# Performance work log

Measured on AMD Instinct MI355X. Metric: run time of the kernel, lower is better.

The kernel has to match this reference:

```python
import math
import jax, jax.numpy as jnp
import numpy as np

B, S, M, H = 8, 2048, 2048, 512
GH = 512  # gate_hidden
MIX_BIAS = -0.25
VARIATION_BIAS = -1.0
PRIOR_SCALE = 1.0
GATE_SCALE = 1.0
GATE_BIAS = 0.0
EPS = 1e-6


def _slerp(a, b, t, eps=EPS):
    # F.normalize semantics: x / max(||x||, eps)
    an = a / jnp.maximum(jnp.linalg.norm(a, axis=-1, keepdims=True), eps)
    bn = b / jnp.maximum(jnp.linalg.norm(b, axis=-1, keepdims=True), eps)
    dot = jnp.clip(jnp.sum(an * bn, axis=-1, keepdims=True), -1.0 + eps, 1.0 - eps)
    omega = jnp.arccos(dot)
    sin_omega = jnp.maximum(jnp.sin(omega), eps)
    t = jnp.clip(t, 0.0, 1.0)
    scale_a = jnp.sin((1.0 - t) * omega) / sin_omega
    scale_b = jnp.sin(t * omega) / sin_omega
    return scale_a * a + scale_b * b


def setup_inputs() -> dict:
    key = jax.random.key(0)
    ks = jax.random.split(key, 20)
    sc = 1.0 / math.sqrt(H)
    sc4 = 1.0 / math.sqrt(4 * H)
    scg = 1.0 / math.sqrt(GH)
    inp = {
        "query": jax.random.normal(ks[0], (B, S, H), jnp.float32),
        "global_anchor": jax.random.normal(ks[1], (B, H), jnp.float32),
        "global_memory": jax.random.normal(ks[2], (B, M, H), jnp.float32),
        "local_absolute": jax.random.normal(ks[3], (B, S, H), jnp.float32),
        "style_context": jax.random.normal(ks[4], (B, S, H), jnp.float32),
        # projection params, stored as [in, out]
        "Wq": jax.random.normal(ks[5], (H, H), jnp.float32) * sc,
        "bq": jnp.zeros((H,), jnp.float32),
        "Wk": jax.random.normal(ks[6], (H, H), jnp.float32) * sc,
        "bk": jnp.zeros((H,), jnp.float32),
        "Wv": jax.random.normal(ks[7], (H, H), jnp.float32) * sc,
        "bv": jnp.zeros((H,), jnp.float32),
        "Wo": jax.random.normal(ks[8], (H, H), jnp.float32) * sc,
        "bo": jnp.zeros((H,), jnp.float32),
        # mix gate MLP: 4H -> GH -> 1
        "Wm1": jax.random.normal(ks[9], (4 * H, GH), jnp.float32) * sc4,
        "bm1": jnp.zeros((GH,), jnp.float32),
        "Wm2": jax.random.normal(ks[10], (GH, 1), jnp.float32) * scg,
        "bm2": jnp.zeros((1,), jnp.float32),
        # variation gate MLP: 4H -> GH -> 1
        "Wg1": jax.random.normal(ks[11], (4 * H, GH), jnp.float32) * sc4,
        "bg1": jnp.zeros((GH,), jnp.float32),
        "Wg2": jax.random.normal(ks[12], (GH, 1), jnp.float32) * scg,
        "bg2": jnp.zeros((1,), jnp.float32),
    }
    return inp


def reference(query, global_anchor, global_memory, local_absolute, style_context,
              Wq, bq, Wk, bk, Wv, bv, Wo, bo,
              Wm1, bm1, Wm2, bm2, Wg1, bg1, Wg2, bg2):
    # expand anchor [B,H] -> [B,S,H]
    anchor_seq = jnp.broadcast_to(global_anchor[:, None, :], query.shape)

    q = query @ Wq + bq                      # [B,S,H]
    k = global_memory @ Wk + bk              # [B,M,H]
    v = global_memory @ Wv + bv              # [B,M,H]

    attn_logits = jnp.einsum('bsh,bmh->bsm', q, k) / math.sqrt(float(H))
    attn = jax.nn.softmax(attn_logits, axis=-1)                      # [B,S,M]
    prior_delta = (jnp.einsum('bsm,bmh->bsh', attn, v) @ Wo + bo) * PRIOR_SCALE
    prior_absolute = anchor_seq + prior_delta

    mix_in = jnp.concatenate([query, prior_absolute, local_absolute, style_context], axis=-1)
    mix_logit = jax.nn.relu(mix_in @ Wm1 + bm1) @ Wm2 + bm2          # [B,S,1]
    mix = jax.nn.sigmoid(mix_logit + MIX_BIAS)

    candidate_absolute = _slerp(prior_absolute, local_absolute, mix)

    var_in = jnp.concatenate([query, candidate_absolute, anchor_seq, style_context], axis=-1)
    variation_logit = jax.nn.relu(var_in @ Wg1 + bg1) @ Wg2 + bg2    # [B,S,1]
    variation_gate = jax.nn.sigmoid(variation_logit * GATE_SCALE + GATE_BIAS + VARIATION_BIAS)

    candidate_delta = candidate_absolute - anchor_seq
    return (attn, prior_delta, prior_absolute, mix, candidate_absolute,
            candidate_delta, variation_logit, variation_gate)
```

## Files before the change

### kernel.cpp

```cpp
#include <hip/hip_runtime.h>
#include <hip/hip_bf16.h>

typedef __hip_bfloat16 bf16;
typedef unsigned short u16;
typedef u16 u16x8 __attribute__((ext_vector_type(8)));
typedef u16 u16x4v __attribute__((ext_vector_type(4)));
typedef short bf16x8 __attribute__((ext_vector_type(8)));
typedef float f32x4 __attribute__((ext_vector_type(4)));

__device__ __forceinline__ float b2f(u16 u) {
    unsigned v = ((unsigned)u) << 16;
    float f; __builtin_memcpy(&f, &v, 4); return f;
}
__device__ __forceinline__ u16 f2u(float f) {
    bf16 h = __float2bfloat16(f);
    u16 u; __builtin_memcpy(&u, &h, 2); return u;
}
__device__ __forceinline__ float sigmoidf_(float x) { return 1.f / (1.f + expf(-x)); }
__device__ __forceinline__ void load8f(const float* __restrict__ p, float* x) {
    float4 a = *reinterpret_cast<const float4*>(p);
    float4 b = *reinterpret_cast<const float4*>(p + 4);
    x[0]=a.x; x[1]=a.y; x[2]=a.z; x[3]=a.w; x[4]=b.x; x[5]=b.y; x[6]=b.z; x[7]=b.w;
}

__device__ __forceinline__ void gld16(const void* g, void* l) {
    typedef __attribute__((address_space(1))) const unsigned int GU;
    typedef __attribute__((address_space(3))) unsigned int LU;
    __builtin_amdgcn_global_load_lds((GU*)(unsigned long long)g,
                                     (LU*)(unsigned int)(unsigned long long)l, 16, 0, 0);
}

template<int EPI, int SWZ>
__global__ __launch_bounds__(256)
void k_mfma(const bf16* __restrict__ A, long long sA, int lda,
            const bf16* __restrict__ Bt, long long sB, int ldb,
            const float* __restrict__ bias, const float* __restrict__ bias2,
            bf16* __restrict__ outb, bf16* __restrict__ outb2, long long sO,
            float* __restrict__ out1, float* __restrict__ out2,
            const float* __restrict__ anchor,
            int N, int K, float scale, int GX)
{
    __shared__ short As[4096];
    __shared__ short Bs[4096];
    const int tid = threadIdx.x;
    const int lin = blockIdx.x;
    int x, y, z;
    if constexpr (SWZ == 0) {
        z = lin & 7; const int t = lin >> 3; x = t % GX; y = t / GX;
    } else {
        const int q = (int)gridDim.x >> 3;
        const int wq = (lin & 7) * q + (lin >> 3);
        x = wq % GX; y = wq / GX; z = 0;
    }
    const int n0 = x * 128, m0 = y * 128;
    const bf16* Az = A + (long long)z * sA;
    const bf16* Bz = Bt + (long long)z * sB;
    const int lrow = tid >> 2;
    const int lcol = (tid & 3) * 8;
    const int lane = tid & 63, w = tid >> 6;
    const int wm = (w >> 1) * 64, wn = (w & 1) * 64;
    const int fr = lane & 15, fq = lane >> 4;
    char* AsW = (char*)As + w * 1024;
    char* BsW = (char*)Bs + w * 1024;

    f32x4 acc[4][4];
#pragma unroll
    for (int i = 0; i < 4; ++i)
#pragma unroll
        for (int j = 0; j < 4; ++j) acc[i][j] = f32x4{0.f, 0.f, 0.f, 0.f};

    for (int k0 = 0; k0 < K; k0 += 32) {
        const bf16* ga = Az + (long long)(m0 + lrow) * lda + (k0 + lcol);
        const bf16* gb = Bz + (long long)(n0 + lrow) * ldb + (k0 + lcol);
        gld16(ga, AsW);
        gld16(ga + 64LL * lda, AsW + 4096);
        gld16(gb, BsW);
        gld16(gb + 64LL * ldb, BsW + 4096);
        __syncthreads();

        bf16x8 af[4], bfr[4];
#pragma unroll
        for (int i = 0; i < 4; ++i)
            af[i] = *reinterpret_cast<const bf16x8*>(&As[(wm + i * 16 + fr) * 32 + fq * 8]);
#pragma unroll
        for (int j = 0; j < 4; ++j)
            bfr[j] = *reinterpret_cast<const bf16x8*>(&Bs[(wn + j * 16 + fr) * 32 + fq * 8]);
#pragma unroll
        for (int i = 0; i < 4; ++i)
#pragma unroll
            for (int j = 0; j < 4; ++j)
                acc[i][j] = __builtin_amdgcn_mfma_f32_16x16x32_bf16(af[i], bfr[j], acc[i][j], 0, 0, 0);
        __syncthreads();
    }

#pragma unroll
    for (int j = 0; j < 4; ++j) {
        const int col = n0 + wn + j * 16 + fr;
        float bv;
        if constexpr (EPI == 1) bv = (col < 512) ? bias[col] : bias2[col - 512];
        else                    bv = bias ? bias[col] : 0.f;
#pragma unroll
        for (int i = 0; i < 4; ++i) {
#pragma unroll
            for (int r = 0; r < 4; ++r) {
                const long long row = m0 + wm + i * 16 + fq * 4 + r;
                const float v = acc[i][j][r];
                if constexpr (EPI == 0) {
                    outb[(long long)z * sO + row * N + col] = __float2bfloat16(v * scale + bv);
                } else if constexpr (EPI == 1) {
                    if (col < 512) outb[row * 512 + col] = __float2bfloat16(v + bv);
                    else           outb2[row * 512 + (col - 512)] = __float2bfloat16(v + bv);
                } else {
                    const float pd = v + bv;
                    const float pa = pd + anchor[(row >> 11) * 512 + col];
                    out1[row * N + col] = pd;
                    out2[row * N + col] = pa;
                    outb[row * N + col] = __float2bfloat16(pa);
                }
            }
        }
    }
}

__global__ __launch_bounds__(256)
void k_softmax_b(bf16* __restrict__ Lb, float* __restrict__ attn)
{
    __shared__ float redm[4], reds[4];
    const long long row = blockIdx.x;
    bf16* lp = Lb + row * 2048;
    float* ap = attn + row * 2048;
    const int tid = threadIdx.x;

    u16x8 u = *reinterpret_cast<const u16x8*>(lp + tid * 8);
    float x[8];
    float mx = -1e30f;
#pragma unroll
    for (int j = 0; j < 8; ++j) { x[j] = b2f(u[j]); mx = fmaxf(mx, x[j]); }
#pragma unroll
    for (int off = 32; off; off >>= 1) mx = fmaxf(mx, __shfl_xor(mx, off));
    if ((tid & 63) == 0) redm[tid >> 6] = mx;
    __syncthreads();
    mx = fmaxf(fmaxf(redm[0], redm[1]), fmaxf(redm[2], redm[3]));

    float s = 0.f;
#pragma unroll
    for (int j = 0; j < 8; ++j) { x[j] = __expf(x[j] - mx); s += x[j]; }
#pragma unroll
    for (int off = 32; off; off >>= 1) s += __shfl_xor(s, off);
    if ((tid & 63) == 0) reds[tid >> 6] = s;
    __syncthreads();
    const float inv = 1.f / (reds[0] + reds[1] + reds[2] + reds[3]);

    u16x8 ob;
#pragma unroll
    for (int j = 0; j < 8; ++j) { x[j] *= inv; ob[j] = f2u(x[j]); }
    *reinterpret_cast<float4*>(ap + tid * 8)     = make_float4(x[0], x[1], x[2], x[3]);
    *reinterpret_cast<float4*>(ap + tid * 8 + 4) = make_float4(x[4], x[5], x[6], x[7]);
    *reinterpret_cast<u16x8*>(lp + tid * 8) = ob;
}

__global__ __launch_bounds__(256)
void k_cat(const bf16* __restrict__ s0b, const bf16* __restrict__ s1b,
           const bf16* __restrict__ s2b, const bf16* __restrict__ s3b,
           int mode2,
           const bf16* __restrict__ Bt, const float* __restrict__ bias,
           const float* __restrict__ w2, float* __restrict__ part)
{
    __shared__ short As[4096];
    __shared__ short Bs[4096];
    __shared__ float pl[128][2];
    const int tid = threadIdx.x;
    const int lin = blockIdx.x;
    const int q = (int)gridDim.x >> 3;
    const int wq = (lin & 7) * q + (lin >> 3);
    const int xt = wq & 3;
    const int n0 = xt * 128, m0 = (wq >> 2) * 128;
    const int lrow = tid >> 2;
    const int lcol = (tid & 3) * 8;
    const int lane = tid & 63, w = tid >> 6;
    const int wm = (w >> 1) * 64, wn = (w & 1) * 64;
    const int fr = lane & 15, fq = lane >> 4;
    char* AsW = (char*)As + w * 1024;
    char* BsW = (char*)Bs + w * 1024;

    f32x4 acc[4][4];
#pragma unroll
    for (int i = 0; i < 4; ++i)
#pragma unroll
        for (int j = 0; j < 4; ++j) acc[i][j] = f32x4{0.f, 0.f, 0.f, 0.f};

    for (int k0 = 0; k0 < 2048; k0 += 32) {
        const int si = k0 >> 9;
        const bf16* sp = si == 0 ? s0b : si == 1 ? s1b : si == 2 ? s2b : s3b;
        const int kloc = (k0 & 511) + lcol;
        const int r = m0 + lrow;
        long long ro0, ro1;
        if (si == 2 && mode2) { ro0 = (long long)(r >> 11) * 512; ro1 = ro0; }
        else                  { ro0 = (long long)r * 512; ro1 = ro0 + 64LL * 512; }
        gld16(sp + ro0 + kloc, AsW);
        gld16(sp + ro1 + kloc, AsW + 4096);
        const bf16* gb = Bt + (long long)(n0 + lrow) * 2048 + (k0 + lcol);
        gld16(gb, BsW);
        gld16(gb + 64LL * 2048, BsW + 4096);
        __syncthreads();

        bf16x8 af[4], bfr[4];
#pragma unroll
        for (int i = 0; i < 4; ++i)
            af[i] = *reinterpret_cast<const bf16x8*>(&As[(wm + i * 16 + fr) * 32 + fq * 8]);
#pragma unroll
        for (int j = 0; j < 4; ++j)
            bfr[j] = *reinterpret_cast<const bf16x8*>(&Bs[(wn + j * 16 + fr) * 32 + fq * 8]);
#pragma unroll
        for (int i = 0; i < 4; ++i)
#pragma unroll
            for (int j = 0; j < 4; ++j)
                acc[i][j] = __builtin_amdgcn_mfma_f32_16x16x32_bf16(af[i], bfr[j], acc[i][j], 0, 0, 0);
        __syncthreads();
    }

    float pt[4][4];
#pragma unroll
    for (int i = 0; i < 4; ++i)
#pragma unroll
        for (int r = 0; r < 4; ++r) pt[i][r] = 0.f;
#pragma unroll
    for (int j = 0; j < 4; ++j) {
        const int col = n0 + wn + j * 16 + fr;
        const float bv = bias[col];
        const float wv = w2[col];
#pragma unroll
        for (int i = 0; i < 4; ++i)
#pragma unroll
            for (int r = 0; r < 4; ++r)
                pt[i][r] = fmaf(fmaxf(acc[i][j][r] + bv, 0.f), wv, pt[i][r]);
    }
#pragma unroll
    for (int off = 1; off < 16; off <<= 1)
#pragma unroll
        for (int i = 0; i < 4; ++i)
#pragma unroll
            for (int r = 0; r < 4; ++r)
                pt[i][r] += __shfl_xor(pt[i][r], off);
    if (fr == 0)
#pragma unroll
        for (int i = 0; i < 4; ++i)
#pragma unroll
            for (int r = 0; r < 4; ++r)
                pl[wm + i * 16 + fq * 4 + r][wn >> 6] = pt[i][r];
    __syncthreads();
    if (tid < 128)
        part[(long long)(m0 + tid) * 4 + xt] = pl[tid][0] + pl[tid][1];
}

__global__ __launch_bounds__(256)
void k_prologue(const float* __restrict__ query, bf16* __restrict__ qb,
                const float* __restrict__ gmem, bf16* __restrict__ gb,
                const float* __restrict__ anchor, bf16* __restrict__ anb,
                const float* Wq, bf16* wtq, const float* Wk, bf16* wtk,
                const float* Wv, bf16* wtv, const float* Wo, bf16* wto,
                const float* Wm1, bf16* wtm1, const float* Wg1, bf16* wtg1)
{
    __shared__ float tls[32][33];
    const int b = blockIdx.x;
    const int tid = threadIdx.x;
    if (b < 8192) {
        const float* s = (b < 4096) ? query : gmem;
        bf16* d = (b < 4096) ? qb : gb;
        const long long i = ((long long)(b & 4095) * 256 + tid) * 8;
        float x[8]; load8f(s + i, x);
        u16x8 o;
#pragma unroll
        for (int j = 0; j < 8; ++j) o[j] = f2u(x[j]);
        *reinterpret_cast<u16x8*>(d + i) = o;
        return;
    }
    if (b < 8194) {
        const int i = ((b - 8192) * 256 + tid) * 8;
        if (i < 4096) {
            float x[8]; load8f(anchor + i, x);
            u16x8 o;
#pragma unroll
            for (int j = 0; j < 8; ++j) o[j] = f2u(x[j]);
            *reinterpret_cast<u16x8*>(anb + i) = o;
        }
        return;
    }
    const float* s; bf16* d; int R, C, ti;
    if (b < 9218) {
        const int bi = b - 8194; const int zz = bi >> 8; ti = bi & 255;
        s = zz == 0 ? Wq : zz == 1 ? Wk : zz == 2 ? Wv : Wo;
        d = zz == 0 ? wtq : zz == 1 ? wtk : zz == 2 ? wtv : wto;
        R = 512; C = 512;
    } else {
        const int bi = b - 9218; const int zz = bi >> 10; ti = bi & 1023;
        s = zz ? Wg1 : Wm1; d = zz ? wtg1 : wtm1;
        R = 2048; C = 512;
    }
    const int c0 = (ti & 15) * 32, r0 = (ti >> 4) * 32;
    const int tr = tid >> 3, tc = (tid & 7) * 4;
    float4 v = *reinterpret_cast<const float4*>(s + (long long)(r0 + tr) * C + c0 + tc);
    tls[tr][tc] = v.x; tls[tr][tc + 1] = v.y; tls[tr][tc + 2] = v.z; tls[tr][tc + 3] = v.w;
    __syncthreads();
    u16x4v o;
    o[0] = f2u(tls[tc + 0][tr]); o[1] = f2u(tls[tc + 1][tr]);
    o[2] = f2u(tls[tc + 2][tr]); o[3] = f2u(tls[tc + 3][tr]);
    *reinterpret_cast<u16x4v*>(d + (long long)(c0 + tr) * R + r0 + tc) = o;
}

__global__ __launch_bounds__(256)
void k_cvt2(const float* __restrict__ s0, bf16* __restrict__ d0,
            const float* __restrict__ s1, bf16* __restrict__ d1)
{
    const int b = blockIdx.x;
    const float* s = (b < 4096) ? s0 : s1;
    bf16* d = (b < 4096) ? d0 : d1;
    const long long i = ((long long)(b & 4095) * 256 + threadIdx.x) * 8;
    float x[8]; load8f(s + i, x);
    u16x8 o;
#pragma unroll
    for (int j = 0; j < 8; ++j) o[j] = f2u(x[j]);
    *reinterpret_cast<u16x8*>(d + i) = o;
}

__global__ __launch_bounds__(256)
void k_trb(const bf16* __restrict__ vb, bf16* __restrict__ vt)
{
    __shared__ u16 t[32][36];
    const int z = blockIdx.z;
    const int h0 = blockIdx.x * 32, s0 = blockIdx.y * 32;
    const int tr = threadIdx.x >> 3, tc = (threadIdx.x & 7) * 4;
    u16x4v a = *reinterpret_cast<const u16x4v*>(
        vb + ((long long)z * 2048 + s0 + tr) * 512 + h0 + tc);
    t[tr][tc] = a[0]; t[tr][tc + 1] = a[1]; t[tr][tc + 2] = a[2]; t[tr][tc + 3] = a[3];
    __syncthreads();
    u16x4v o;
    o[0] = t[tc + 0][tr]; o[1] = t[tc + 1][tr]; o[2] = t[tc + 2][tr]; o[3] = t[tc + 3][tr];
    *reinterpret_cast<u16x4v*>(
        vt + (long long)z * 1048576 + (long long)(h0 + tr) * 2048 + s0 + tc) = o;
}

__global__ __launch_bounds__(64)
void k_gate_slerp(const float* __restrict__ part, const float* __restrict__ b2,
                  const bf16* __restrict__ priorb, const bf16* __restrict__ localb,
                  const float* __restrict__ anchor,
                  float* __restrict__ o_mix,
                  float* __restrict__ cand, float* __restrict__ cdelta,
                  bf16* __restrict__ candb)
{
    const int row = blockIdx.x;
    const int lane = threadIdx.x;
    float v = (lane < 4) ? part[(long long)row * 4 + lane] : 0.f;
    v += __shfl_xor(v, 1);
    v += __shfl_xor(v, 2);
    const float logit = __shfl(v, 0) + b2[0];
    float t = sigmoidf_(logit - 0.25f);
    if (lane == 0) o_mix[row] = t;
    t = fminf(fmaxf(t, 0.f), 1.f);

    const long long base = (long long)row * 512 + lane * 8;
    const long long abase = (long long)(row >> 11) * 512 + lane * 8;
    u16x8 ua = *reinterpret_cast<const u16x8*>(priorb + base);
    u16x8 ub = *reinterpret_cast<const u16x8*>(localb + base);
    float a[8], b[8];
    float sa = 0.f, sb = 0.f, sab = 0.f;
#pragma unroll
    for (int j = 0; j < 8; ++j) {
        a[j] = b2f(ua[j]); b[j] = b2f(ub[j]);
        sa = fmaf(a[j], a[j], sa); sb = fmaf(b[j], b[j], sb); sab = fmaf(a[j], b[j], sab);
    }
#pragma unroll
    for (int off = 1; off < 64; off <<= 1) {
        sa += __shfl_xor(sa, off); sb += __shfl_xor(sb, off); sab += __shfl_xor(sab, off);
    }
    const float eps = 1e-6f;
    float na = fmaxf(sqrtf(sa), eps), nb = fmaxf(sqrtf(sb), eps);
    float dot = sab / (na * nb);
    dot = fminf(fmaxf(dot, -1.f + eps), 1.f - eps);
    float omega = acosf(dot);
    float so = fmaxf(sinf(omega), eps);
    float sca = sinf((1.f - t) * omega) / so;
    float scb = sinf(t * omega) / so;

    float an[8];
    load8f(anchor + abase, an);
    float c0[8], d0[8];
    u16x8 cb;
#pragma unroll
    for (int j = 0; j < 8; ++j) {
        c0[j] = sca * a[j] + scb * b[j];
        d0[j] = c0[j] - an[j];
        cb[j] = f2u(c0[j]);
    }
    *reinterpret_cast<float4*>(cand + base)       = make_float4(c0[0], c0[1], c0[2], c0[3]);
    *reinterpret_cast<float4*>(cand + base + 4)   = make_float4(c0[4], c0[5], c0[6], c0[7]);
    *reinterpret_cast<float4*>(cdelta + base)     = make_float4(d0[0], d0[1], d0[2], d0[3]);
    *reinterpret_cast<float4*>(cdelta + base + 4) = make_float4(d0[4], d0[5], d0[6], d0[7]);
    *reinterpret_cast<u16x8*>(candb + base) = cb;
}

__global__ __launch_bounds__(256)
void k_gate_var(const float* __restrict__ part, const float* __restrict__ b2,
                float* __restrict__ o_vl, float* __restrict__ o_vg)
{
    const long long row = (long long)blockIdx.x * 256 + threadIdx.x;
    float4 p = *reinterpret_cast<const float4*>(part + row * 4);
    const float logit = (p.x + p.y) + (p.z + p.w) + b2[0];
    o_vl[row] = logit;
    o_vg[row] = sigmoidf_(logit - 1.0f);
}

extern "C" void kernel_launch(void* const* d_in, const int* in_sizes, int n_in,
                              void* d_out, int out_size, void* d_ws, size_t ws_size,
                              hipStream_t stream)
{
    const float* query  = (const float*)d_in[0];
    const float* anchor = (const float*)d_in[1];
    const float* gmem   = (const float*)d_in[2];
    const float* local_ = (const float*)d_in[3];
    const float* style  = (const float*)d_in[4];
    const float* Wq = (const float*)d_in[5];   const float* bq = (const float*)d_in[6];
    const float* Wk = (const float*)d_in[7];   const float* bk = (const float*)d_in[8];
    const float* Wv = (const float*)d_in[9];   const float* bv = (const float*)d_in[10];
    const float* Wo = (const float*)d_in[11];  const float* bo = (const float*)d_in[12];
    const float* Wm1 = (const float*)d_in[13]; const float* bm1 = (const float*)d_in[14];
    const float* Wm2 = (const float*)d_in[15]; const float* bm2 = (const float*)d_in[16];
    const float* Wg1 = (const float*)d_in[17]; const float* bg1 = (const float*)d_in[18];
    const float* Wg2 = (const float*)d_in[19]; const float* bg2 = (const float*)d_in[20];

    float* out = (float*)d_out;
    const long long SHE = 8388608LL;
    float* o_attn = out;
    float* o_pd   = out + 33554432LL;
    float* o_pa   = o_pd + SHE;
    float* o_mix  = o_pa + SHE;
    float* o_ca   = o_mix + 16384;
    float* o_cd   = o_ca + SHE;
    float* o_vl   = o_cd + SHE;
    float* o_vg   = o_vl + 16384;

    bf16* S0q = (bf16*)d_ws;
    bf16* S1  = S0q + SHE;
    bf16* S2  = S1 + SHE;
    bf16* S3  = S2 + SHE;
    bf16* S4  = S3 + SHE;
    bf16* wtq = S4 + SHE;
    bf16* wtk = wtq + 262144;
    bf16* wtv = wtk + 262144;
    bf16* wto = wtv + 262144;
    bf16* wtm1 = wto + 262144;
    bf16* wtg1 = wtm1 + 1048576;
    bf16* anb  = wtg1 + 1048576;
    float* part_m = (float*)(anb + 4096);
    float* part_v = part_m + 65536;
    bf16* p_b  = (bf16*)o_ca;
    bf16* v_b  = (bf16*)o_ca;

    const float invSqrtH = 0.04419417382415922f;

    k_prologue<<<11266, 256, 0, stream>>>(query, S0q, gmem, S1, anchor, anb,
        Wq, wtq, Wk, wtk, Wv, wtv, Wo, wto, Wm1, wtm1, Wg1, wtg1);
    k_mfma<0, 1><<<512, 256, 0, stream>>>(S0q, 0, 512, wtq, 0, 512, bq, nullptr,
        S2, nullptr, 0, nullptr, nullptr, nullptr, 512, 512, 1.f, 4);
    k_mfma<1, 1><<<1024, 256, 0, stream>>>(S1, 0, 512, wtk, 0, 512, bk, bv,
        S3, v_b, 0, nullptr, nullptr, nullptr, 1024, 512, 1.f, 8);
    k_trb<<<dim3(16, 64, 8), 256, 0, stream>>>(v_b, S4);
    k_mfma<0, 0><<<2048, 256, 0, stream>>>(S2, 2048LL * 512, 512, S3, 2048LL * 512, 512,
        nullptr, nullptr, p_b, nullptr, 4194304LL, nullptr, nullptr, nullptr,
        2048, 512, invSqrtH, 16);
    k_softmax_b<<<16384, 256, 0, stream>>>(p_b, o_attn);
    k_mfma<0, 0><<<512, 256, 0, stream>>>(p_b, 4194304LL, 2048, S4, 1048576LL, 2048,
        nullptr, nullptr, S1, nullptr, 1048576LL, nullptr, nullptr, nullptr,
        512, 2048, 1.f, 4);
    k_cvt2<<<8192, 256, 0, stream>>>(local_, S3, style, S4);
    k_mfma<2, 1><<<512, 256, 0, stream>>>(S1, 0, 512, wto, 0, 512, bo, nullptr,
        S2, nullptr, 0, o_pd, o_pa, anchor, 512, 512, 1.f, 4);
    k_cat<<<512, 256, 0, stream>>>(S0q, S2, S3, S4, 0, wtm1, bm1, Wm2, part_m);
    k_gate_slerp<<<16384, 64, 0, stream>>>(part_m, bm2, S2, S3, anchor,
        o_mix, o_ca, o_cd, S2);
    k_cat<<<512, 256, 0, stream>>>(S0q, S2, anb, S4, 1, wtg1, bg1, Wg2, part_v);
    k_gate_var<<<64, 256, 0, stream>>>(part_v, bg2, o_vl, o_vg);
}
```

Measured before the change: 430.8 us.

## Merge independent GEMM and elementwise launches into combined kernels, use nontemporal stores

Merges the Q and K/V projections into one launch, runs the V transpose alongside the QK^T GEMM, and runs the local/style bf16 conversion alongside the Wo projection, with the block index choosing the role. This cuts kernel launches and the idle tails between dependent kernels. The V staging buffer moves to the attn output region so the transpose and the QK^T GEMM do not clash over memory. Large fp32 output writes (attn, prior delta/absolute, candidate outputs) now use nontemporal stores to reduce cache pollution. Heterogeneous blocks in one grid may balance unevenly.

```diff
diff --git a/kernel.cpp b/kernel.cpp
--- a/kernel.cpp
+++ b/kernel.cpp
@@ -22,6 +22,13 @@
     float4 b = *reinterpret_cast<const float4*>(p + 4);
     x[0]=a.x; x[1]=a.y; x[2]=a.z; x[3]=a.w; x[4]=b.x; x[5]=b.y; x[6]=b.z; x[7]=b.w;
 }
+__device__ __forceinline__ void nt_store4(float* p, float a, float b, float c, float d) {
+    f32x4 v = {a, b, c, d};
+    __builtin_nontemporal_store(v, reinterpret_cast<f32x4*>(p));
+}
+__device__ __forceinline__ void nt_store1(float* p, float a) {
+    __builtin_nontemporal_store(a, p);
+}
 
 __device__ __forceinline__ void gld16(const void* g, void* l) {
     typedef __attribute__((address_space(1))) const unsigned int GU;
@@ -31,24 +38,21 @@
 }
 
 template<int EPI, int SWZ>
-__global__ __launch_bounds__(256)
-void k_mfma(const bf16* __restrict__ A, long long sA, int lda,
-            const bf16* __restrict__ Bt, long long sB, int ldb,
-            const float* __restrict__ bias, const float* __restrict__ bias2,
-            bf16* __restrict__ outb, bf16* __restrict__ outb2, long long sO,
-            float* __restrict__ out1, float* __restrict__ out2,
-            const float* __restrict__ anchor,
-            int N, int K, float scale, int GX)
-{
-    __shared__ short As[4096];
-    __shared__ short Bs[4096];
+__device__ __forceinline__ void mfma_core(
+    int lin, int nwg, short* As, short* Bs,
+    const bf16* A, long long sA, int lda,
+    const bf16* Bt, long long sB, int ldb,
+    const float* bias, const float* bias2,
+    bf16* outb, bf16* outb2, long long sO,
+    float* out1, float* out2, const float* anchor,
+    int N, int K, float scale, int GX)
+{
     const int tid = threadIdx.x;
-    const int lin = blockIdx.x;
     int x, y, z;
     if constexpr (SWZ == 0) {
         z = lin & 7; const int t = lin >> 3; x = t % GX; y = t / GX;
     } else {
-        const int q = (int)gridDim.x >> 3;
+        const int q = nwg >> 3;
         const int wq = (lin & 7) * q + (lin >> 3);
         x = wq % GX; y = wq / GX; z = 0;
     }
@@ -113,12 +117,101 @@
                 } else {
                     const float pd = v + bv;
                     const float pa = pd + anchor[(row >> 11) * 512 + col];
-                    out1[row * N + col] = pd;
-                    out2[row * N + col] = pa;
+                    nt_store1(&out1[row * N + col], pd);
+                    nt_store1(&out2[row * N + col], pa);
                     outb[row * N + col] = __float2bfloat16(pa);
                 }
             }
         }
+    }
+}
+
+__global__ __launch_bounds__(256)
+void k_pv(const bf16* __restrict__ Pb, const bf16* __restrict__ Vt,
+          bf16* __restrict__ ctx)
+{
+    __shared__ short SH[8192];
+    mfma_core<0, 0>(blockIdx.x, 512, SH, SH + 4096,
+                    Pb, 4194304LL, 2048, Vt, 1048576LL, 2048,
+                    nullptr, nullptr, ctx, nullptr, 1048576LL,
+                    nullptr, nullptr, nullptr, 512, 2048, 1.f, 4);
+}
+
+__global__ __launch_bounds__(256)
+void k_proj(const bf16* __restrict__ S0q, const bf16* __restrict__ wtq,
+            const float* __restrict__ bq, bf16* __restrict__ S2,
+            const bf16* __restrict__ S1, const bf16* __restrict__ wtk,
+            const float* __restrict__ bk, const float* __restrict__ bv,
+            bf16* __restrict__ S3, bf16* __restrict__ v_b)
+{
+    __shared__ short SH[8192];
+    const int b = blockIdx.x;
+    if (b < 512) {
+        mfma_core<0, 1>(b, 512, SH, SH + 4096,
+                        S0q, 0, 512, wtq, 0, 512, bq, nullptr,
+                        S2, nullptr, 0, nullptr, nullptr, nullptr,
+                        512, 512, 1.f, 4);
+    } else {
+        mfma_core<1, 1>(b - 512, 1024, SH, SH + 4096,
+                        S1, 0, 512, wtk, 0, 512, bk, bv,
+                        S3, v_b, 0, nullptr, nullptr, nullptr,
+                        1024, 512, 1.f, 8);
+    }
+}
+
+__global__ __launch_bounds__(256)
+void k_qkt_trb(const bf16* __restrict__ v_b, bf16* __restrict__ vt,
+               const bf16* __restrict__ S2q, const bf16* __restrict__ S3k,
+               bf16* __restrict__ p_b, float scale)
+{
+    __shared__ short SH[8192];
+    const int b = blockIdx.x;
+    if (b < 8192) {
+        u16 (*t)[36] = (u16(*)[36])SH;
+        const int z = b >> 10;
+        const int bi = b & 1023;
+        const int h0 = (bi & 15) * 32, s0 = (bi >> 4) * 32;
+        const int tr = threadIdx.x >> 3, tc = (threadIdx.x & 7) * 4;
+        u16x4v a = *reinterpret_cast<const u16x4v*>(
+            v_b + ((long long)z * 2048 + s0 + tr) * 512 + h0 + tc);
+        t[tr][tc] = a[0]; t[tr][tc + 1] = a[1]; t[tr][tc + 2] = a[2]; t[tr][tc + 3] = a[3];
+        __syncthreads();
+        u16x4v o;
+        o[0] = t[tc + 0][tr]; o[1] = t[tc + 1][tr]; o[2] = t[tc + 2][tr]; o[3] = t[tc + 3][tr];
+        *reinterpret_cast<u16x4v*>(
+            vt + (long long)z * 1048576 + (long long)(h0 + tr) * 2048 + s0 + tc) = o;
+    } else {
+        mfma_core<0, 0>(b - 8192, 2048, SH, SH + 4096,
+                        S2q, 2048LL * 512, 512, S3k, 2048LL * 512, 512,
+                        nullptr, nullptr, p_b, nullptr, 4194304LL,
+                        nullptr, nullptr, nullptr, 2048, 512, scale, 16);
+    }
+}
+
+__global__ __launch_bounds__(256)
+void k_wo_cvt(const float* __restrict__ local_, bf16* __restrict__ S3d,
+              const float* __restrict__ style, bf16* __restrict__ S4d,
+              const bf16* __restrict__ S1ctx, const bf16* __restrict__ wto,
+              const float* __restrict__ bo, bf16* __restrict__ S2pa,
+              float* __restrict__ o_pd, float* __restrict__ o_pa,
+              const float* __restrict__ anchor)
+{
+    __shared__ short SH[8192];
+    const int b = blockIdx.x;
+    if (b < 8192) {
+        const float* s = (b < 4096) ? local_ : style;
+        bf16* d = (b < 4096) ? S3d : S4d;
+        const long long i = ((long long)(b & 4095) * 256 + threadIdx.x) * 8;
+        float x[8]; load8f(s + i, x);
+        u16x8 o;
+#pragma unroll
+        for (int j = 0; j < 8; ++j) o[j] = f2u(x[j]);
+        *reinterpret_cast<u16x8*>(d + i) = o;
+    } else {
+        mfma_core<2, 1>(b - 8192, 512, SH, SH + 4096,
+                        S1ctx, 0, 512, wto, 0, 512, bo, nullptr,
+                        S2pa, nullptr, 0, o_pd, o_pa, anchor,
+                        512, 512, 1.f, 4);
     }
 }
 
@@ -154,8 +247,8 @@
     u16x8 ob;
 #pragma unroll
     for (int j = 0; j < 8; ++j) { x[j] *= inv; ob[j] = f2u(x[j]); }
-    *reinterpret_cast<float4*>(ap + tid * 8)     = make_float4(x[0], x[1], x[2], x[3]);
-    *reinterpret_cast<float4*>(ap + tid * 8 + 4) = make_float4(x[4], x[5], x[6], x[7]);
+    nt_store4(ap + tid * 8,     x[0], x[1], x[2], x[3]);
+    nt_store4(ap + tid * 8 + 4, x[4], x[5], x[6], x[7]);
     *reinterpret_cast<u16x8*>(lp + tid * 8) = ob;
 }
 
@@ -308,38 +401,6 @@
     *reinterpret_cast<u16x4v*>(d + (long long)(c0 + tr) * R + r0 + tc) = o;
 }
 
-__global__ __launch_bounds__(256)
-void k_cvt2(const float* __restrict__ s0, bf16* __restrict__ d0,
-            const float* __restrict__ s1, bf16* __restrict__ d1)
-{
-    const int b = blockIdx.x;
-    const float* s = (b < 4096) ? s0 : s1;
-    bf16* d = (b < 4096) ? d0 : d1;
-    const long long i = ((long long)(b & 4095) * 256 + threadIdx.x) * 8;
-    float x[8]; load8f(s + i, x);
-    u16x8 o;
-#pragma unroll
-    for (int j = 0; j < 8; ++j) o[j] = f2u(x[j]);
-    *reinterpret_cast<u16x8*>(d + i) = o;
-}
-
-__global__ __launch_bounds__(256)
-void k_trb(const bf16* __restrict__ vb, bf16* __restrict__ vt)
-{
-    __shared__ u16 t[32][36];
-    const int z = blockIdx.z;
-    const int h0 = blockIdx.x * 32, s0 = blockIdx.y * 32;
-    const int tr = threadIdx.x >> 3, tc = (threadIdx.x & 7) * 4;
-    u16x4v a = *reinterpret_cast<const u16x4v*>(
-        vb + ((long long)z * 2048 + s0 + tr) * 512 + h0 + tc);
-    t[tr][tc] = a[0]; t[tr][tc + 1] = a[1]; t[tr][tc + 2] = a[2]; t[tr][tc + 3] = a[3];
-    __syncthreads();
-    u16x4v o;
-    o[0] = t[tc + 0][tr]; o[1] = t[tc + 1][tr]; o[2] = t[tc + 2][tr]; o[3] = t[tc + 3][tr];
-    *reinterpret_cast<u16x4v*>(
-        vt + (long long)z * 1048576 + (long long)(h0 + tr) * 2048 + s0 + tc) = o;
-}
-
 __global__ __launch_bounds__(64)
 void k_gate_slerp(const float* __restrict__ part, const float* __restrict__ b2,
                   const bf16* __restrict__ priorb, const bf16* __restrict__ localb,
@@ -392,10 +453,10 @@
         d0[j] = c0[j] - an[j];
         cb[j] = f2u(c0[j]);
     }
-    *reinterpret_cast<float4*>(cand + base)       = make_float4(c0[0], c0[1], c0[2], c0[3]);
-    *reinterpret_cast<float4*>(cand + base + 4)   = make_float4(c0[4], c0[5], c0[6], c0[7]);
-    *reinterpret_cast<float4*>(cdelta + base)     = make_float4(d0[0], d0[1], d0[2], d0[3]);
-    *reinterpret_cast<float4*>(cdelta + base + 4) = make_float4(d0[4], d0[5], d0[6], d0[7]);
+    nt_store4(cand + base,       c0[0], c0[1], c0[2], c0[3]);
+    nt_store4(cand + base + 4,   c0[4], c0[5], c0[6], c0[7]);
+    nt_store4(cdelta + base,     d0[0], d0[1], d0[2], d0[3]);
+    nt_store4(cdelta + base + 4, d0[4], d0[5], d0[6], d0[7]);
     *reinterpret_cast<u16x8*>(candb + base) = cb;
 }
 
@@ -454,27 +515,18 @@
     float* part_m = (float*)(anb + 4096);
     float* part_v = part_m + 65536;
     bf16* p_b  = (bf16*)o_ca;
-    bf16* v_b  = (bf16*)o_ca;
+    bf16* v_b  = (bf16*)o_attn;
 
     const float invSqrtH = 0.04419417382415922f;
 
     k_prologue<<<11266, 256, 0, stream>>>(query, S0q, gmem, S1, anchor, anb,
         Wq, wtq, Wk, wtk, Wv, wtv, Wo, wto, Wm1, wtm1, Wg1, wtg1);
-    k_mfma<0, 1><<<512, 256, 0, stream>>>(S0q, 0, 512, wtq, 0, 512, bq, nullptr,
-        S2, nullptr, 0, nullptr, nullptr, nullptr, 512, 512, 1.f, 4);
-    k_mfma<1, 1><<<1024, 256, 0, stream>>>(S1, 0, 512, wtk, 0, 512, bk, bv,
-        S3, v_b, 0, nullptr, nullptr, nullptr, 1024, 512, 1.f, 8);
-    k_trb<<<dim3(16, 64, 8), 256, 0, stream>>>(v_b, S4);
-    k_mfma<0, 0><<<2048, 256, 0, stream>>>(S2, 2048LL * 512, 512, S3, 2048LL * 512, 512,
-        nullptr, nullptr, p_b, nullptr, 4194304LL, nullptr, nullptr, nullptr,
-        2048, 512, invSqrtH, 16);
+    k_proj<<<1536, 256, 0, stream>>>(S0q, wtq, bq, S2, S1, wtk, bk, bv, S3, v_b);
+    k_qkt_trb<<<10240, 256, 0, stream>>>(v_b, S4, S2, S3, p_b, invSqrtH);
     k_softmax_b<<<16384, 256, 0, stream>>>(p_b, o_attn);
-    k_mfma<0, 0><<<512, 256, 0, stream>>>(p_b, 4194304LL, 2048, S4, 1048576LL, 2048,
-        nullptr, nullptr, S1, nullptr, 1048576LL, nullptr, nullptr, nullptr,
-        512, 2048, 1.f, 4);
-    k_cvt2<<<8192, 256, 0, stream>>>(local_, S3, style, S4);
-    k_mfma<2, 1><<<512, 256, 0, stream>>>(S1, 0, 512, wto, 0, 512, bo, nullptr,
-        S2, nullptr, 0, o_pd, o_pa, anchor, 512, 512, 1.f, 4);
+    k_pv<<<512, 256, 0, stream>>>(p_b, S4, S1);
+    k_wo_cvt<<<8704, 256, 0, stream>>>(local_, S3, style, S4, S1, wto, bo,
+        S2, o_pd, o_pa, anchor);
     k_cat<<<512, 256, 0, stream>>>(S0q, S2, S3, S4, 0, wtm1, bm1, Wm2, part_m);
     k_gate_slerp<<<16384, 64, 0, stream>>>(part_m, bm2, S2, S3, anchor,
         o_mix, o_ca, o_cd, S2);
```

Result: faster. 396.0 us (-8.1%).
